# Optimization experiments

Measured on AMD Instinct MI355X. Metric: run time of the kernel, lower is better.

## Reference

```python
import jax, jax.numpy as jnp
import numpy as np

OUT_F = 4096
IN_F = 4096
NUM_BITS = 4
BLOCK = 64
R = 16
LORA_SCALE = 32.0 / R  # lora_alpha / r


def setup_inputs() -> dict:
    key = jax.random.key(0)
    k1, k2, k3, k4, k5, k6 = jax.random.split(key, 6)
    n_packed = OUT_F * IN_F * NUM_BITS // 8  # bytes; 2 nibbles per byte
    n_blocks = OUT_F * IN_F // BLOCK
    return {
        "x": jax.random.normal(k1, (2, 1024, IN_F), dtype=jnp.float32),
        "qweight": jax.random.randint(k2, (n_packed,), 0, 256, dtype=jnp.int32),
        "scales": jax.random.uniform(k3, (n_blocks,), dtype=jnp.float32),
        "bias": jax.random.normal(k4, (OUT_F,), dtype=jnp.float32),
        "lora_A": jax.random.normal(k5, (R, IN_F), dtype=jnp.float32) * 0.02,
        "lora_B": jax.random.normal(k6, (OUT_F, R), dtype=jnp.float32) * 0.02,
    }


def _dequantize(qweight, scales):
    # uniform 4-bit lookup table: linspace(-1, 1, 16)
    table = jnp.linspace(-1.0, 1.0, 2 ** NUM_BITS).astype(scales.dtype)
    mask = (1 << NUM_BITS) - 1
    # unpack: index i stored at bits [i*NUM_BITS, (i+1)*NUM_BITS) of each byte
    lo = qweight & mask
    hi = (qweight >> NUM_BITS) & mask
    idx = jnp.stack([lo, hi], axis=-1).reshape(-1)  # [OUT_F*IN_F]
    vals = table[idx]                                # gather from lookup table
    # per-block rescale, then reshape to [OUT_F, IN_F]
    w = vals.reshape(-1, BLOCK) * scales[:, None]
    return w.reshape(OUT_F, IN_F)


def reference(x, qweight, scales, bias, lora_A, lora_B):
    W = _dequantize(qweight, scales)                      # [out, in]
    base = jnp.einsum('bsi,oi->bso', x, W) + bias          # F.linear
    lora = jnp.einsum('bsr,or->bso', jnp.einsum('bsi,ri->bsr', x, lora_A), lora_B)
    return base + LORA_SCALE * lora
```

## Files before the change

kernel.cpp:

```cpp
#include <hip/hip_runtime.h>
#include <hip/hip_bf16.h>
#include <stdint.h>

#define IN_F   4096
#define OUT_F  4096
#define M_ROWS 2048
#define LORA_SCALE 2.0f

typedef __bf16 bf16x8 __attribute__((ext_vector_type(8)));
typedef float  f32x4  __attribute__((ext_vector_type(4)));

typedef const __attribute__((address_space(1))) void gvoid_t;
typedef __attribute__((address_space(3))) void lvoid_t;

__global__ void prep_kernel(const int* __restrict__ qw,
                            const float* __restrict__ scales,
                            __hip_bfloat16* __restrict__ W,
                            const float* __restrict__ x,
                            __hip_bfloat16* __restrict__ xb,
                            const float* __restrict__ A,
                            float* __restrict__ tout) {
    int b = blockIdx.x;
    if (b < 512) {
        __shared__ float red[16 * 4 * 16];
        int m0 = b * 4;
        int r = threadIdx.x & 15;
        int g = threadIdx.x >> 4;
        float acc[4] = {0.f, 0.f, 0.f, 0.f};
        for (int kb = 0; kb < 64; ++kb) {
            int k = kb * 64 + g * 4;
            float4 av = *(const float4*)(A + (size_t)r * IN_F + k);
            #pragma unroll
            for (int row = 0; row < 4; ++row) {
                float4 xv = *(const float4*)(x + (size_t)(m0 + row) * IN_F + k);
                acc[row] += xv.x*av.x + xv.y*av.y + xv.z*av.z + xv.w*av.w;
            }
        }
        #pragma unroll
        for (int row = 0; row < 4; ++row) red[g*64 + row*16 + r] = acc[row];
        __syncthreads();
        if (threadIdx.x < 64) {
            int row = threadIdx.x >> 4, rr = threadIdx.x & 15;
            float s = 0.f;
            #pragma unroll
            for (int gg = 0; gg < 16; ++gg) s += red[gg*64 + row*16 + rr];
            tout[(size_t)(m0 + row) * 16 + rr] = s;
        }
    } else if (b < 8704) {
        int t = (b - 512) * 256 + threadIdx.x;
        int4 q = ((const int4*)qw)[t];
        float scale = scales[t >> 3];
        float step = scale * (2.0f / 15.0f);
        int bb[4] = {q.x, q.y, q.z, q.w};
        union { __hip_bfloat16 h[8]; uint4 v; } o;
        #pragma unroll
        for (int j = 0; j < 4; ++j) {
            float lo = (float)(bb[j] & 15)        * step - scale;
            float hi = (float)((bb[j] >> 4) & 15) * step - scale;
            o.h[2*j]   = __float2bfloat16(lo);
            o.h[2*j+1] = __float2bfloat16(hi);
        }
        ((uint4*)W)[t] = o.v;
    } else {
        int t = (b - 8704) * 256 + threadIdx.x;
        float4 a = ((const float4*)x)[2*t];
        float4 c = ((const float4*)x)[2*t + 1];
        union { __hip_bfloat16 h[8]; uint4 v; } o;
        o.h[0] = __float2bfloat16(a.x); o.h[1] = __float2bfloat16(a.y);
        o.h[2] = __float2bfloat16(a.z); o.h[3] = __float2bfloat16(a.w);
        o.h[4] = __float2bfloat16(c.x); o.h[5] = __float2bfloat16(c.y);
        o.h[6] = __float2bfloat16(c.z); o.h[7] = __float2bfloat16(c.w);
        ((uint4*)xb)[t] = o.v;
    }
}

__global__ __launch_bounds__(256) void gemm_kernel(
        const __hip_bfloat16* __restrict__ A,
        const __hip_bfloat16* __restrict__ B,
        float* __restrict__ out0,
        float* __restrict__ p1) {
    const int K = IN_F, N = OUT_F;
    __shared__ __hip_bfloat16 As[2][128*32];
    __shared__ __hip_bfloat16 Bs[2][128*32];

    int tid  = threadIdx.x;
    int wave = tid >> 6, lane = tid & 63;
    int wm = wave >> 1, wn = wave & 1;
    int row16 = lane & 15, quad = lane >> 4;
    int m0 = blockIdx.y * 128, n0 = blockIdx.x * 128;
    int kb = blockIdx.z * 2048;

    int rl = lane >> 2;
    int cg = (lane & 3) ^ ((rl >> 1) & 3);

    const __hip_bfloat16* pA0 = A + (size_t)(m0 + wave*32 + rl) * K + kb + cg*8;
    const __hip_bfloat16* pA1 = pA0 + (size_t)16 * K;
    const __hip_bfloat16* pB0 = B + (size_t)(n0 + wave*32 + rl) * K + kb + cg*8;
    const __hip_bfloat16* pB1 = pB0 + (size_t)16 * K;

    lvoid_t* dA0[2] = { (lvoid_t*)&As[0][(wave*2+0)*512], (lvoid_t*)&As[1][(wave*2+0)*512] };
    lvoid_t* dA1[2] = { (lvoid_t*)&As[0][(wave*2+1)*512], (lvoid_t*)&As[1][(wave*2+1)*512] };
    lvoid_t* dB0[2] = { (lvoid_t*)&Bs[0][(wave*2+0)*512], (lvoid_t*)&Bs[1][(wave*2+0)*512] };
    lvoid_t* dB1[2] = { (lvoid_t*)&Bs[0][(wave*2+1)*512], (lvoid_t*)&Bs[1][(wave*2+1)*512] };

    f32x4 acc[4][4];
    #pragma unroll
    for (int i = 0; i < 4; ++i)
        #pragma unroll
        for (int j = 0; j < 4; ++j) acc[i][j] = (f32x4){0.f, 0.f, 0.f, 0.f};

    #define COMPUTE(buf)                                                          \
    {                                                                             \
        bf16x8 af[4], bfr[4];                                                     \
        _Pragma("unroll")                                                         \
        for (int mt = 0; mt < 4; ++mt) {                                          \
            int row = wm*64 + mt*16 + row16;                                      \
            af[mt] = *(const bf16x8*)&As[buf][row*32 + ((quad ^ ((row>>1)&3)) << 3)]; \
        }                                                                         \
        _Pragma("unroll")                                                         \
        for (int nt = 0; nt < 4; ++nt) {                                          \
            int row = wn*64 + nt*16 + row16;                                      \
            bfr[nt] = *(const bf16x8*)&Bs[buf][row*32 + ((quad ^ ((row>>1)&3)) << 3)]; \
        }                                                                         \
        _Pragma("unroll")                                                         \
        for (int mt = 0; mt < 4; ++mt)                                            \
            _Pragma("unroll")                                                     \
            for (int nt = 0; nt < 4; ++nt)                                        \
                acc[mt][nt] = __builtin_amdgcn_mfma_f32_16x16x32_bf16(            \
                    af[mt], bfr[nt], acc[mt][nt], 0, 0, 0);                       \
    }

    #define DMA(buf)                                                              \
        __builtin_amdgcn_global_load_lds((gvoid_t*)pA0, dA0[buf], 16, 0, 0);      \
        __builtin_amdgcn_global_load_lds((gvoid_t*)pA1, dA1[buf], 16, 0, 0);      \
        __builtin_amdgcn_global_load_lds((gvoid_t*)pB0, dB0[buf], 16, 0, 0);      \
        __builtin_amdgcn_global_load_lds((gvoid_t*)pB1, dB1[buf], 16, 0, 0);      \
        pA0 += 32; pA1 += 32; pB0 += 32; pB1 += 32;

    DMA(0)
    __syncthreads();

    for (int i = 0; i < 31; ++i) {
        DMA(1)
        COMPUTE(0)
        __syncthreads();
        DMA(0)
        COMPUTE(1)
        __syncthreads();
    }
    DMA(1)
    COMPUTE(0)
    __syncthreads();
    COMPUTE(1)

    #undef COMPUTE
    #undef DMA

    float* dst = blockIdx.z ? p1 : out0;
    #pragma unroll
    for (int nt = 0; nt < 4; ++nt) {
        int n = n0 + wn*64 + nt*16 + row16;
        #pragma unroll
        for (int mt = 0; mt < 4; ++mt) {
            #pragma unroll
            for (int r = 0; r < 4; ++r) {
                int ml = wm*64 + mt*16 + quad*4 + r;
                dst[(size_t)(m0 + ml) * N + n] = acc[mt][nt][r];
            }
        }
    }
}

__global__ __launch_bounds__(256) void epilogue_kernel(
        float* __restrict__ out, const float* __restrict__ p1,
        const float* __restrict__ bias, const float* __restrict__ loraB,
        const float* __restrict__ tmat) {
    const int N = OUT_F;
    __shared__ float tl[16 * 16];
    int m0 = blockIdx.y * 16, n0 = blockIdx.x * 64;
    int tid = threadIdx.x;
    if (tid < 64) ((float4*)tl)[tid] = ((const float4*)(tmat + (size_t)m0 * 16))[tid];
    __syncthreads();

    int nl = tid & 63, mq = tid >> 6;
    int n = n0 + nl;
    const float4* lb = (const float4*)(loraB + (size_t)n * 16);
    float4 b0 = lb[0], b1 = lb[1], b2 = lb[2], b3 = lb[3];
    float bn = bias[n];

    #pragma unroll
    for (int j = 0; j < 4; ++j) {
        int ml = mq * 4 + j;
        const float* tm = &tl[ml * 16];
        float dot =
            tm[0]*b0.x + tm[1]*b0.y + tm[2]*b0.z + tm[3]*b0.w +
            tm[4]*b1.x + tm[5]*b1.y + tm[6]*b1.z + tm[7]*b1.w +
            tm[8]*b2.x + tm[9]*b2.y + tm[10]*b2.z + tm[11]*b2.w +
            tm[12]*b3.x + tm[13]*b3.y + tm[14]*b3.z + tm[15]*b3.w;
        size_t off = (size_t)(m0 + ml) * N + n;
        out[off] = out[off] + p1[off] + bn + LORA_SCALE * dot;
    }
}

extern "C" void kernel_launch(void* const* d_in, const int* in_sizes, int n_in,
                              void* d_out, int out_size, void* d_ws, size_t ws_size,
                              hipStream_t stream) {
    const float* x      = (const float*)d_in[0];
    const int*   qw     = (const int*)d_in[1];
    const float* scales = (const float*)d_in[2];
    const float* bias   = (const float*)d_in[3];
    const float* loraA  = (const float*)d_in[4];
    const float* loraB  = (const float*)d_in[5];
    float* out = (float*)d_out;

    char* ws = (char*)d_ws;
    __hip_bfloat16* Wb = (__hip_bfloat16*)ws;
    __hip_bfloat16* Xb = (__hip_bfloat16*)(ws + 33554432);
    float* tmat        = (float*)(ws + 50331648);
    float* p1          = (float*)(ws + 50462720);

    prep_kernel    <<<12800, 256, 0, stream>>>(qw, scales, Wb, x, Xb, loraA, tmat);
    gemm_kernel    <<<dim3(32, 16, 2), 256, 0, stream>>>(Xb, Wb, out, p1);
    epilogue_kernel<<<dim3(64, 128), 256, 0, stream>>>(out, p1, bias, loraB, tmat);
}
```

Before: 264.3 us.

## Fuse epilogue into GEMM, drop split-K, use 4-stage LDS pipeline

The separate bias/LoRA epilogue kernel is folded into the GEMM kernel's store phase, reading tmat through shared memory reused via a union. The split-K over two z-slices is removed, so no partial-sum buffer is written and re-read. The double-buffered K loop becomes a 4-stage ring with explicit vmcnt waits and raw barriers, which keeps more loads in flight. The cost is half as many workgroups (512 on a large-CU device), twice the K length per block, and larger LDS use that may reduce occupancy.

```diff
diff --git a/kernel.cpp b/kernel.cpp
--- a/kernel.cpp
+++ b/kernel.cpp
@@ -12,6 +12,8 @@
 
 typedef const __attribute__((address_space(1))) void gvoid_t;
 typedef __attribute__((address_space(3))) void lvoid_t;
+
+#define WAITVM(n) __builtin_amdgcn_s_waitcnt(((n)&0xF) | (((n)>>4)<<14) | (7<<4) | (15<<8))
 
 __global__ void prep_kernel(const int* __restrict__ qw,
                             const float* __restrict__ scales,
@@ -77,37 +79,42 @@
 __global__ __launch_bounds__(256) void gemm_kernel(
         const __hip_bfloat16* __restrict__ A,
         const __hip_bfloat16* __restrict__ B,
-        float* __restrict__ out0,
-        float* __restrict__ p1) {
+        const float* __restrict__ bias,
+        const float* __restrict__ loraB,
+        const float* __restrict__ tmat,
+        float* __restrict__ out) {
     const int K = IN_F, N = OUT_F;
-    __shared__ __hip_bfloat16 As[2][128*32];
-    __shared__ __hip_bfloat16 Bs[2][128*32];
+    __shared__ union alignas(16) {
+        struct { __hip_bfloat16 As[4][128*32]; __hip_bfloat16 Bs[4][128*32]; } s;
+        float tl[128 * 16];
+    } sm;
 
     int tid  = threadIdx.x;
     int wave = tid >> 6, lane = tid & 63;
     int wm = wave >> 1, wn = wave & 1;
     int row16 = lane & 15, quad = lane >> 4;
     int m0 = blockIdx.y * 128, n0 = blockIdx.x * 128;
-    int kb = blockIdx.z * 2048;
 
     int rl = lane >> 2;
     int cg = (lane & 3) ^ ((rl >> 1) & 3);
 
-    const __hip_bfloat16* pA0 = A + (size_t)(m0 + wave*32 + rl) * K + kb + cg*8;
+    const __hip_bfloat16* pA0 = A + (size_t)(m0 + wave*32 + rl) * K + cg*8;
     const __hip_bfloat16* pA1 = pA0 + (size_t)16 * K;
-    const __hip_bfloat16* pB0 = B + (size_t)(n0 + wave*32 + rl) * K + kb + cg*8;
+    const __hip_bfloat16* pB0 = B + (size_t)(n0 + wave*32 + rl) * K + cg*8;
     const __hip_bfloat16* pB1 = pB0 + (size_t)16 * K;
-
-    lvoid_t* dA0[2] = { (lvoid_t*)&As[0][(wave*2+0)*512], (lvoid_t*)&As[1][(wave*2+0)*512] };
-    lvoid_t* dA1[2] = { (lvoid_t*)&As[0][(wave*2+1)*512], (lvoid_t*)&As[1][(wave*2+1)*512] };
-    lvoid_t* dB0[2] = { (lvoid_t*)&Bs[0][(wave*2+0)*512], (lvoid_t*)&Bs[1][(wave*2+0)*512] };
-    lvoid_t* dB1[2] = { (lvoid_t*)&Bs[0][(wave*2+1)*512], (lvoid_t*)&Bs[1][(wave*2+1)*512] };
 
     f32x4 acc[4][4];
     #pragma unroll
     for (int i = 0; i < 4; ++i)
         #pragma unroll
         for (int j = 0; j < 4; ++j) acc[i][j] = (f32x4){0.f, 0.f, 0.f, 0.f};
+
+    #define DMA(buf)                                                              \
+        __builtin_amdgcn_global_load_lds((gvoid_t*)pA0, (lvoid_t*)&sm.s.As[buf][(wave*2+0)*512], 16, 0, 0); \
+        __builtin_amdgcn_global_load_lds((gvoid_t*)pA1, (lvoid_t*)&sm.s.As[buf][(wave*2+1)*512], 16, 0, 0); \
+        __builtin_amdgcn_global_load_lds((gvoid_t*)pB0, (lvoid_t*)&sm.s.Bs[buf][(wave*2+0)*512], 16, 0, 0); \
+        __builtin_amdgcn_global_load_lds((gvoid_t*)pB1, (lvoid_t*)&sm.s.Bs[buf][(wave*2+1)*512], 16, 0, 0); \
+        pA0 += 32; pA1 += 32; pB0 += 32; pB1 += 32;
 
     #define COMPUTE(buf)                                                          \
     {                                                                             \
@@ -115,12 +122,12 @@
         _Pragma("unroll")                                                         \
         for (int mt = 0; mt < 4; ++mt) {                                          \
             int row = wm*64 + mt*16 + row16;                                      \
-            af[mt] = *(const bf16x8*)&As[buf][row*32 + ((quad ^ ((row>>1)&3)) << 3)]; \
+            af[mt] = *(const bf16x8*)&sm.s.As[buf][row*32 + ((quad ^ ((row>>1)&3)) << 3)]; \
         }                                                                         \
         _Pragma("unroll")                                                         \
         for (int nt = 0; nt < 4; ++nt) {                                          \
             int row = wn*64 + nt*16 + row16;                                      \
-            bfr[nt] = *(const bf16x8*)&Bs[buf][row*32 + ((quad ^ ((row>>1)&3)) << 3)]; \
+            bfr[nt] = *(const bf16x8*)&sm.s.Bs[buf][row*32 + ((quad ^ ((row>>1)&3)) << 3)]; \
         }                                                                         \
         _Pragma("unroll")                                                         \
         for (int mt = 0; mt < 4; ++mt)                                            \
@@ -130,75 +137,61 @@
                     af[mt], bfr[nt], acc[mt][nt], 0, 0, 0);                       \
     }
 
-    #define DMA(buf)                                                              \
-        __builtin_amdgcn_global_load_lds((gvoid_t*)pA0, dA0[buf], 16, 0, 0);      \
-        __builtin_amdgcn_global_load_lds((gvoid_t*)pA1, dA1[buf], 16, 0, 0);      \
-        __builtin_amdgcn_global_load_lds((gvoid_t*)pB0, dB0[buf], 16, 0, 0);      \
-        __builtin_amdgcn_global_load_lds((gvoid_t*)pB1, dB1[buf], 16, 0, 0);      \
-        pA0 += 32; pA1 += 32; pB0 += 32; pB1 += 32;
+    #define STEP(p)                                                               \
+        WAITVM(8);                                  \
+        __builtin_amdgcn_s_barrier();       \
+        __builtin_amdgcn_sched_barrier(0);                                        \
+        COMPUTE(p)                                                                \
+        DMA((p+3)&3)
 
     DMA(0)
-    __syncthreads();
-
-    for (int i = 0; i < 31; ++i) {
-        DMA(1)
-        COMPUTE(0)
-        __syncthreads();
-        DMA(0)
-        COMPUTE(1)
-        __syncthreads();
-    }
     DMA(1)
-    COMPUTE(0)
-    __syncthreads();
+    DMA(2)
+
+    for (int u = 0; u < 31; ++u) {
+        STEP(0)
+        STEP(1)
+        STEP(2)
+        STEP(3)
+    }
+    STEP(0)
+    WAITVM(8); __builtin_amdgcn_s_barrier(); __builtin_amdgcn_sched_barrier(0);
     COMPUTE(1)
-
+    WAITVM(4); __builtin_amdgcn_s_barrier(); __builtin_amdgcn_sched_barrier(0);
+    COMPUTE(2)
+    WAITVM(0); __builtin_amdgcn_s_barrier(); __builtin_amdgcn_sched_barrier(0);
+    COMPUTE(3)
+
+    #undef STEP
     #undef COMPUTE
     #undef DMA
 
-    float* dst = blockIdx.z ? p1 : out0;
+    #pragma unroll
+    for (int i = 0; i < 2; ++i)
+        ((float4*)sm.tl)[tid + i*256] =
+            ((const float4*)(tmat + (size_t)m0 * 16))[tid + i*256];
+    __syncthreads();
+
     #pragma unroll
     for (int nt = 0; nt < 4; ++nt) {
         int n = n0 + wn*64 + nt*16 + row16;
+        float bn = bias[n];
+        const float4* lb = (const float4*)(loraB + (size_t)n * 16);
+        float4 b0 = lb[0], b1 = lb[1], b2 = lb[2], b3 = lb[3];
         #pragma unroll
         for (int mt = 0; mt < 4; ++mt) {
             #pragma unroll
             for (int r = 0; r < 4; ++r) {
                 int ml = wm*64 + mt*16 + quad*4 + r;
-                dst[(size_t)(m0 + ml) * N + n] = acc[mt][nt][r];
+                const float* tm = &sm.tl[ml * 16];
+                float dot =
+                    tm[0]*b0.x + tm[1]*b0.y + tm[2]*b0.z + tm[3]*b0.w +
+                    tm[4]*b1.x + tm[5]*b1.y + tm[6]*b1.z + tm[7]*b1.w +
+                    tm[8]*b2.x + tm[9]*b2.y + tm[10]*b2.z + tm[11]*b2.w +
+                    tm[12]*b3.x + tm[13]*b3.y + tm[14]*b3.z + tm[15]*b3.w;
+                out[(size_t)(m0 + ml) * N + n] = acc[mt][nt][r] + bn + LORA_SCALE * dot;
             }
         }
-    }
-}
-
-__global__ __launch_bounds__(256) void epilogue_kernel(
-        float* __restrict__ out, const float* __restrict__ p1,
-        const float* __restrict__ bias, const float* __restrict__ loraB,
-        const float* __restrict__ tmat) {
-    const int N = OUT_F;
-    __shared__ float tl[16 * 16];
-    int m0 = blockIdx.y * 16, n0 = blockIdx.x * 64;
-    int tid = threadIdx.x;
-    if (tid < 64) ((float4*)tl)[tid] = ((const float4*)(tmat + (size_t)m0 * 16))[tid];
-    __syncthreads();
-
-    int nl = tid & 63, mq = tid >> 6;
-    int n = n0 + nl;
-    const float4* lb = (const float4*)(loraB + (size_t)n * 16);
-    float4 b0 = lb[0], b1 = lb[1], b2 = lb[2], b3 = lb[3];
-    float bn = bias[n];
-
-    #pragma unroll
-    for (int j = 0; j < 4; ++j) {
-        int ml = mq * 4 + j;
-        const float* tm = &tl[ml * 16];
-        float dot =
-            tm[0]*b0.x + tm[1]*b0.y + tm[2]*b0.z + tm[3]*b0.w +
-            tm[4]*b1.x + tm[5]*b1.y + tm[6]*b1.z + tm[7]*b1.w +
-            tm[8]*b2.x + tm[9]*b2.y + tm[10]*b2.z + tm[11]*b2.w +
-            tm[12]*b3.x + tm[13]*b3.y + tm[14]*b3.z + tm[15]*b3.w;
-        size_t off = (size_t)(m0 + ml) * N + n;
-        out[off] = out[off] + p1[off] + bn + LORA_SCALE * dot;
     }
 }
 
@@ -217,9 +210,7 @@
     __hip_bfloat16* Wb = (__hip_bfloat16*)ws;
     __hip_bfloat16* Xb = (__hip_bfloat16*)(ws + 33554432);
     float* tmat        = (float*)(ws + 50331648);
-    float* p1          = (float*)(ws + 50462720);
-
-    prep_kernel    <<<12800, 256, 0, stream>>>(qw, scales, Wb, x, Xb, loraA, tmat);
-    gemm_kernel    <<<dim3(32, 16, 2), 256, 0, stream>>>(Xb, Wb, out, p1);
-    epilogue_kernel<<<dim3(64, 128), 256, 0, stream>>>(out, p1, bias, loraB, tmat);
+
+    prep_kernel<<<12800, 256, 0, stream>>>(qw, scales, Wb, x, Xb, loraA, tmat);
+    gemm_kernel<<<dim3(32, 16), 256, 0, stream>>>(Xb, Wb, bias, loraB, tmat, out);
 }
```

New measurement: 261.8 us. No clear change (-0.9%).
